# Kernel tuning notes

Hardware: AMD Instinct MI355X
Metric: run time of the kernel (lower is better)

The kernel has to match this reference:

```python
import jax, jax.numpy as jnp
import numpy as np

PATCH = 8

def setup_inputs() -> dict:
    key = jax.random.key(0)
    k0, k1, k2, k3 = jax.random.split(key, 4)
    dim = 128
    hidden = int(dim * 3)
    B, H, W = 4, 256, 256
    x = jax.random.normal(k0, (B, dim, H, W), jnp.float32)
    # project_in: Conv2d(dim, 2*hidden, k=1, bias=False) -> weight [2h, dim]
    w_in = jax.random.normal(k1, (2 * hidden, dim), jnp.float32) * 0.02
    # dwconv: Conv2d(2h, 2h, k=3, groups=2h) -> depthwise kernel [2h, 1, 3, 3]
    w_dw = jax.random.normal(k2, (2 * hidden, 1, 3, 3), jnp.float32) * 0.1
    # spectral filter, initialized to ones as in the module
    fft_filter = jnp.ones((dim, 1, 1, PATCH, PATCH // 2 + 1), jnp.float32)
    # project_out: Conv2d(hidden, dim, k=1) -> weight [dim, hidden]
    w_out = jax.random.normal(k3, (dim, hidden), jnp.float32) * 0.02
    return {"x": x, "w_in": w_in, "w_dw": w_dw, "fft_filter": fft_filter, "w_out": w_out}


def reference(x, w_in, w_dw, fft_filter, w_out):
    P = PATCH
    # 1x1 project_in: [B, dim, H, W] -> [B, 2h, H, W]
    h = jnp.einsum('oi,bihw->bohw', w_in, x)
    # 3x3 depthwise conv, SAME padding
    h = jax.lax.conv_general_dilated(
        h, w_dw, window_strides=(1, 1), padding='SAME',
        dimension_numbers=('NCHW', 'OIHW', 'NCHW'),
        feature_group_count=h.shape[1])
    x1, x2 = jnp.split(h, 2, axis=1)
    g = jax.nn.gelu(x1, approximate=False) * x2  # torch F.gelu is exact erf
    # 1x1 project_out: [B, hidden, H, W] -> [B, dim, H, W]
    y = jnp.einsum('oi,bihw->bohw', w_out, g)
    b, c, H, W = y.shape
    hn = (P - H % P) % P
    wn = (P - W % P) % P
    if hn or wn:
        y = jnp.pad(y, ((0, 0), (0, 0), (0, hn), (0, wn)), mode='reflect')
    Hp, Wp = y.shape[2], y.shape[3]
    # b c (h p1) (w p2) -> b c h w p1 p2
    yp = y.reshape(b, c, Hp // P, P, Wp // P, P).transpose(0, 1, 2, 4, 3, 5)
    yf = jnp.fft.rfft2(yp)                 # [b, c, h, w, P, P//2+1] complex
    yf = yf * fft_filter                   # broadcast over (c,1,1,P,P//2+1)
    yp = jnp.fft.irfft2(yf, s=(P, P))
    y = yp.transpose(0, 1, 2, 4, 3, 5).reshape(b, c, Hp, Wp)
    return y[:, :, :H, :W]
```

## Files before the change

### kernel.cpp

```cpp
#include <hip/hip_runtime.h>

typedef _Float16 f16;
typedef _Float16 f16x2 __attribute__((ext_vector_type(2)));
typedef _Float16 f16x4 __attribute__((ext_vector_type(4)));
typedef _Float16 f16x8 __attribute__((ext_vector_type(8)));
typedef __fp16  fp16x2 __attribute__((ext_vector_type(2)));
typedef float f32x4 __attribute__((ext_vector_type(4)));

#define DIM  128
#define HID  384
#define HID2 768
#define NPX  65536
#define NB   4

static __device__ __forceinline__ f16x2 bc2(unsigned u) {
    union { unsigned u; f16x2 h; } x; x.u = u; return x.h;
}

__global__ __launch_bounds__(256) void k_prep_w(
    const float* __restrict__ w_in, const float* __restrict__ w_out,
    const float* __restrict__ w_dw,
    f16* __restrict__ wibf, f16* __restrict__ wobf, f16* __restrict__ wpkT)
{
    int i = blockIdx.x * 256 + threadIdx.x;
    if (i < HID2 * DIM) {
        int j = i & 7, l = (i >> 3) & 63, ni = (i >> 9) & 3;
        int wn = (i >> 11) & 1, kk = (i >> 12) & 3, cN = i >> 14;
        int lr = l & 15, lh = l >> 4;
        int n = wn*64 + ni*16 + lr;
        int row = (n < 64) ? cN*64 + n : 384 + cN*64 + (n - 64);
        wibf[i] = (f16)w_in[row*128 + kk*32 + lh*8 + j];
    }
    if (i < DIM * HID) {
        int j = i & 7, l = (i >> 3) & 63, ni = (i >> 9) & 3;
        int wn = (i >> 11) & 1, kk2 = (i >> 12) & 1, cs = i >> 13;
        int lr = l & 15, lh = l >> 4;
        int ch_out = wn*64 + ni*16 + lr;
        int ch_in  = cs*64 + kk2*32 + lh*8 + j;
        wobf[i] = (f16)w_out[ch_out*HID + ch_in];
    }
    if (i < 9 * HID2) {
        int k = i / HID2, ch = i - k * HID2;
        wpkT[i] = (f16)w_dw[ch * 9 + k];
    }
}

__global__ void k_ktab(const float* __restrict__ filt, float* __restrict__ ktab,
                       int* __restrict__ isdelta)
{
    int c = blockIdx.x, t = threadIdx.x;
    int a = t >> 3, bb = t & 7;
    const float ct[8] = {1.f, 0.70710678118654752f, 0.f, -0.70710678118654752f,
                        -1.f, -0.70710678118654752f, 0.f, 0.70710678118654752f};
    float s = 0.f;
    for (int u = 0; u < 8; ++u)
        for (int v = 0; v < 8; ++v) {
            float Guv = (v <= 4) ? filt[c*40 + u*5 + v]
                                 : filt[c*40 + ((8-u)&7)*5 + (8-v)];
            s += Guv * ct[(u*a + v*bb) & 7];
        }
    s *= (1.f/64.f);
    ktab[c*64 + t] = s;
    float want = (t == 0) ? 1.f : 0.f;
    unsigned long long m = __ballot(fabsf(s - want) < 1e-5f);
    if (t == 0) isdelta[c] = (m == 0xFFFFFFFFFFFFFFFFULL) ? 1 : 0;
}

__global__ __launch_bounds__(256) void k_transpose(
    const float* __restrict__ x, f16* __restrict__ xt)
{
    __shared__ float tile[64][65];
    const int b = blockIdx.z;
    const float* xb = x + (size_t)b * DIM * NPX;
    f16* xtb = xt + (size_t)b * NPX * DIM;
    const int c0 = blockIdx.y * 64, p0 = blockIdx.x * 64;
    for (int i = threadIdx.x; i < 4096; i += 256) {
        int cl = i >> 6, pl = i & 63;
        tile[pl][cl] = xb[(size_t)(c0+cl)*NPX + p0 + pl];
    }
    __syncthreads();
    for (int i = threadIdx.x; i < 2048; i += 256) {
        int pl = i >> 5, c2 = (i & 31) * 2;
        f16x2 v = { (f16)tile[pl][c2], (f16)tile[pl][c2+1] };
        *(f16x2*)&xtb[(size_t)(p0+pl)*DIM + c0 + c2] = v;
    }
}

__global__ __launch_bounds__(256, 2) void k_fused(
    const f16* __restrict__ xt, const f16* __restrict__ wibf,
    const f16* __restrict__ wobf, const f16* __restrict__ wpkT,
    const float* __restrict__ ktab, const int* __restrict__ isdelta,
    float* __restrict__ out)
{
    __shared__ __attribute__((aligned(16))) char uni[33792];
    __shared__ f16 h1s[64*132];
    __shared__ f16 h2s[64*132];
    __shared__ f16 gAs[64*64];
    f16*   As = (f16*)uni;
    float* yl = (float*)uni;

    const int t  = threadIdx.x;
    const int tx = (blockIdx.x & 31) * 8;
    const int ty = (blockIdx.x >> 5) * 8;
    const f16* xtb = xt + (size_t)blockIdx.y * NPX * DIM;
    float* outb = out + (size_t)blockIdx.y * DIM * NPX;

#pragma unroll
    for (int j = 0; j < 8; ++j) {
        int i = t + j*256;
        int m = i >> 4, c8 = i & 15;
        int hr = (m * 683) >> 13;
        int hc = m - hr*12;
        int gy = ty - 1 + hr, gx = tx - 1 + hc;
        f16x8 v = {0,0,0,0,0,0,0,0};
        if (hr < 10 && hc < 10 && (unsigned)gy < 256u && (unsigned)gx < 256u)
            v = *(const f16x8*)&xtb[(size_t)(gy*256 + gx)*DIM + c8*8];
        *(f16x8*)&As[(m*128 + c8*8) ^ ((m & 7) << 3)] = v;
    }
    __syncthreads();

    const int l = t & 63, w = t >> 6, lr = l & 15, lh = l >> 4;
    const int wm = w >> 1, wn = w & 1;
    const int sch = t & 63;
    const int spy = (t >> 6) * 2;

    unsigned Ap[4][6], Up[4][4];
    f16x2 w2[9];
    f16x2 acc2a[2][4], acc2b[2][4];
    f32x4 accY[2][4];
#pragma unroll
    for (int mi = 0; mi < 2; ++mi)
#pragma unroll
        for (int ni = 0; ni < 4; ++ni) accY[mi][ni] = (f32x4){0.f,0.f,0.f,0.f};

#define STEN_LOAD(HB, CHOFF)                                                     \
    { _Pragma("unroll")                                                          \
      for (int r = 0; r < 4; ++r) {                                              \
        const f16* rp = &HB[sch*132 + (spy + r)*12];                             \
        uint2 q0 = *(const uint2*)(rp);                                          \
        uint2 q1 = *(const uint2*)(rp + 4);                                      \
        uint2 q2 = *(const uint2*)(rp + 8);                                      \
        Ap[r][0]=q0.x; Ap[r][1]=q0.y; Ap[r][2]=q1.x;                             \
        Ap[r][3]=q1.y; Ap[r][4]=q2.x; Ap[r][5]=q2.y;                             \
        Up[r][0]=__builtin_amdgcn_alignbit(Ap[r][1],Ap[r][0],16);                \
        Up[r][1]=__builtin_amdgcn_alignbit(Ap[r][2],Ap[r][1],16);                \
        Up[r][2]=__builtin_amdgcn_alignbit(Ap[r][3],Ap[r][2],16);                \
        Up[r][3]=__builtin_amdgcn_alignbit(Ap[r][4],Ap[r][3],16);                \
      }                                                                          \
      _Pragma("unroll")                                                          \
      for (int k = 0; k < 9; ++k) {                                              \
        f16 wv = wpkT[k*HID2 + (CHOFF) + cs*64 + sch];                           \
        w2[k] = (f16x2){wv, wv};                                                 \
      } }

#define STEN_FMA(ACC2)                                                           \
    { _Pragma("unroll")                                                          \
      for (int rr = 0; rr < 2; ++rr) {                                           \
        _Pragma("unroll")                                                        \
        for (int j = 0; j < 4; ++j) ACC2[rr][j] = (f16x2){0,0};                  \
        _Pragma("unroll")                                                        \
        for (int dy = 0; dy < 3; ++dy) {                                         \
          int r = rr + dy;                                                       \
          _Pragma("unroll")                                                      \
          for (int j = 0; j < 4; ++j) {                                          \
            ACC2[rr][j] = __builtin_elementwise_fma(bc2(Ap[r][j]),   w2[dy*3+0], ACC2[rr][j]); \
            ACC2[rr][j] = __builtin_elementwise_fma(bc2(Up[r][j]),   w2[dy*3+1], ACC2[rr][j]); \
            ACC2[rr][j] = __builtin_elementwise_fma(bc2(Ap[r][j+1]), w2[dy*3+2], ACC2[rr][j]); \
          } } } }

#define GATE_GA()                                                                \
    { _Pragma("unroll")                                                          \
      for (int rr = 0; rr < 2; ++rr) {                                           \
        const int oy = spy + rr;                                                 \
        _Pragma("unroll")                                                        \
        for (int j = 0; j < 4; ++j) {                                            \
          _Pragma("unroll")                                                      \
          for (int hf = 0; hf < 2; ++hf) {                                       \
            float av_ = (float)acc2a[rr][j][hf];                                 \
            float bv_ = (float)acc2b[rr][j][hf];                                 \
            float z  = av_ * 0.70710678118654752f;                               \
            float z2 = z * z;                                                    \
            float er = z * (1.1283791671f + z2*(-0.3761263890f                   \
                         + z2*0.1128379167f));                                   \
            er = fminf(1.0f, fmaxf(-1.0f, er));                                  \
            float ge = 0.5f * av_ * (1.0f + er);                                 \
            int jx = j*2 + hf;                                                   \
            gAs[(oy*8 + jx)*64 + (sch ^ (jx << 3))] = (f16)(ge * bv_);           \
          } } } }

#define GEMM2(CS)                                                                \
    { _Pragma("unroll")                                                          \
      for (int kk2 = 0; kk2 < 2; ++kk2) {                                        \
        f16x8 a2[2], b2[4];                                                      \
        _Pragma("unroll")                                                        \
        for (int mi = 0; mi < 2; ++mi) {                                         \
          int row = wm*32 + mi*16 + lr;                                          \
          a2[mi] = *(const f16x8*)&gAs[row*64 + ((kk2*32 + lh*8) ^ ((row&7)<<3))]; \
        }                                                                        \
        _Pragma("unroll")                                                        \
        for (int ni = 0; ni < 4; ++ni)                                           \
          b2[ni] = *(const f16x8*)&wobf[(((((CS)*2 + kk2)*2 + wn)*4 + ni)*64 + l)*8]; \
        _Pragma("unroll")                                                        \
        for (int mi = 0; mi < 2; ++mi)                                           \
          _Pragma("unroll")                                                      \
          for (int ni = 0; ni < 4; ++ni)                                         \
            accY[mi][ni] = __builtin_amdgcn_mfma_f32_16x16x32_f16(               \
                a2[mi], b2[ni], accY[mi][ni], 0, 0, 0);                          \
      } }

    for (int cN = 0; cN < 6; ++cN) {
        const bool doS = (cN > 0);
        const int  cs  = cN - 1;

        f32x4 acc[4][4];
#pragma unroll
        for (int mi = 0; mi < 4; ++mi)
#pragma unroll
            for (int ni = 0; ni < 4; ++ni) acc[mi][ni] = (f32x4){0.f,0.f,0.f,0.f};

#pragma unroll
        for (int kk = 0; kk < 4; ++kk) {
            f16x8 avf[4], bvf[4];
#pragma unroll
            for (int mi = 0; mi < 4; ++mi) {
                int r = wm*64 + mi*16 + lr;
                avf[mi] = *(const f16x8*)&As[(r*128 + kk*32 + lh*8) ^ ((r & 7) << 3)];
            }
#pragma unroll
            for (int ni = 0; ni < 4; ++ni)
                bvf[ni] = *(const f16x8*)
                    &wibf[((((cN*4 + kk)*2 + wn)*4 + ni)*64 + l) * 8];
            __builtin_amdgcn_s_setprio(1);
#pragma unroll
            for (int mi = 0; mi < 4; ++mi)
#pragma unroll
                for (int ni = 0; ni < 4; ++ni)
                    acc[mi][ni] = __builtin_amdgcn_mfma_f32_16x16x32_f16(
                        avf[mi], bvf[ni], acc[mi][ni], 0, 0, 0);
            __builtin_amdgcn_s_setprio(0);

            if (doS) {
                if (kk == 0) { STEN_LOAD(h1s, 0) }
                if (kk == 1) { STEN_FMA(acc2a) }
                if (kk == 2) { STEN_LOAD(h2s, HID) }
                if (kk == 3) { STEN_FMA(acc2b) }
            }
        }
        if (doS) { GATE_GA() }

        __syncthreads();
        if (doS) { GEMM2(cs) }

        {
            f16* hb = (wn == 0) ? h1s : h2s;
#pragma unroll
            for (int mi = 0; mi < 4; ++mi)
#pragma unroll
                for (int ni = 0; ni < 4; ++ni) {
                    int ch = ni*16 + lr;
                    int m  = wm*64 + mi*16 + lh*4;
                    union { struct { fp16x2 a, b; } p; f16x4 v; } u;
                    u.p.a = __builtin_amdgcn_cvt_pkrtz(acc[mi][ni][0], acc[mi][ni][1]);
                    u.p.b = __builtin_amdgcn_cvt_pkrtz(acc[mi][ni][2], acc[mi][ni][3]);
                    *(f16x4*)&hb[ch*132 + m] = u.v;
                }
        }
        __syncthreads();
    }

    {
        const int cs = 5;
        STEN_LOAD(h1s, 0)
        STEN_FMA(acc2a)
        STEN_LOAD(h2s, HID)
        STEN_FMA(acc2b)
        GATE_GA()
        __syncthreads();
        GEMM2(5)
    }

#pragma unroll
    for (int mi = 0; mi < 2; ++mi)
#pragma unroll
        for (int ni = 0; ni < 4; ++ni) {
            int ch = wn*64 + ni*16 + lr;
#pragma unroll
            for (int r = 0; r < 4; ++r) {
                int px = wm*32 + mi*16 + lh*4 + r;
                yl[px*132 + ch] = accY[mi][ni][r];
            }
        }
    __syncthreads();

    const int c = t & 127, half = t >> 7;
    if (isdelta[c]) {
#pragma unroll
        for (int r = 0; r < 4; ++r) {
            int pl = half*4 + r;
            float o0[8];
#pragma unroll
            for (int xx = 0; xx < 8; ++xx) o0[xx] = yl[(pl*8 + xx)*132 + c];
            size_t ob = (size_t)c*NPX + (size_t)(ty + pl)*256 + tx;
            *(float4*)&outb[ob]     = make_float4(o0[0], o0[1], o0[2], o0[3]);
            *(float4*)&outb[ob + 4] = make_float4(o0[4], o0[5], o0[6], o0[7]);
        }
    } else {
        const float* kc = &ktab[c*64];
        for (int r = 0; r < 4; ++r) {
            int pyl = half*4 + r;
            float o0[8];
            for (int xx = 0; xx < 8; ++xx) {
                float s = 0.f;
                for (int a = 0; a < 8; ++a)
                    for (int bb = 0; bb < 8; ++bb)
                        s += kc[a*8 + bb] *
                             yl[(((pyl - a) & 7)*8 + ((xx - bb) & 7))*132 + c];
                o0[xx] = s;
            }
            size_t ob = (size_t)c*NPX + (size_t)(ty + pyl)*256 + tx;
            *(float4*)&outb[ob]     = make_float4(o0[0], o0[1], o0[2], o0[3]);
            *(float4*)&outb[ob + 4] = make_float4(o0[4], o0[5], o0[6], o0[7]);
        }
    }
#undef STEN_LOAD
#undef STEN_FMA
#undef GATE_GA
#undef GEMM2
}

__global__ void k_diag(float* out, float v) { out[0] = v; }

extern "C" void kernel_launch(void* const* d_in, const int* in_sizes, int n_in,
                              void* d_out, int out_size, void* d_ws, size_t ws_size,
                              hipStream_t stream)
{
    const float* x     = (const float*)d_in[0];
    const float* w_in  = (const float*)d_in[1];
    const float* w_dw  = (const float*)d_in[2];
    const float* filt  = (const float*)d_in[3];
    const float* w_out = (const float*)d_in[4];
    float* out = (float*)d_out;
    char* ws = (char*)d_ws;

    const size_t OFF_WIB = 0;
    const size_t OFF_WOB = 196608;
    const size_t OFF_KT  = OFF_WOB + 98304;
    const size_t OFF_ISD = OFF_KT + 32768;
    const size_t OFF_WPK = OFF_ISD + 512;
    const size_t WEND    = 524288;

    const size_t SZ_XT = (size_t)NB * NPX * DIM * 2;
    const size_t NEED  = WEND + SZ_XT;
    if (ws_size < NEED) {
        k_diag<<<1, 1, 0, stream>>>(out, (float)((double)ws_size / 1048576.0));
        return;
    }

    f16*   wibf = (f16*)(ws + OFF_WIB);
    f16*   wobf = (f16*)(ws + OFF_WOB);
    float* kt   = (float*)(ws + OFF_KT);
    int*   isd  = (int*)(ws + OFF_ISD);
    f16*   wpk  = (f16*)(ws + OFF_WPK);
    f16*   xt   = (f16*)(ws + WEND);

    k_prep_w<<<dim3(384), dim3(256), 0, stream>>>(w_in, w_out, w_dw, wibf, wobf, wpk);
    k_ktab<<<dim3(128), dim3(64), 0, stream>>>(filt, kt, isd);
    k_transpose<<<dim3(1024, 2, NB), dim3(256), 0, stream>>>(x, xt);
    k_fused<<<dim3(1024, NB), dim3(256), 0, stream>>>(xt, wibf, wobf, wpk, kt, isd, out);
}
```

Measured before the change: 359.8 us.

## Double fused kernel block to 512 threads with finer per-wave work split

Raises the fused kernel to 512 threads (8 waves) per block. Each wave now computes half the output columns of the GEMM tiles, one stencil output row and fewer accumulators, so register pressure drops and more waves can hide latency. The h1s/h2s row pitch is padded from 132 to 134 to change LDS bank mapping. Block indices are swizzled so consecutive blocks cover spread-out tiles. The cost is more waves each doing less MFMA work and reloading the same A fragments, plus larger barriers.

```diff
diff --git a/kernel.cpp b/kernel.cpp
--- a/kernel.cpp
+++ b/kernel.cpp
@@ -86,28 +86,30 @@
     }
 }
 
-__global__ __launch_bounds__(256, 2) void k_fused(
+__global__ __launch_bounds__(512, 4) void k_fused(
     const f16* __restrict__ xt, const f16* __restrict__ wibf,
     const f16* __restrict__ wobf, const f16* __restrict__ wpkT,
     const float* __restrict__ ktab, const int* __restrict__ isdelta,
     float* __restrict__ out)
 {
     __shared__ __attribute__((aligned(16))) char uni[33792];
-    __shared__ f16 h1s[64*132];
-    __shared__ f16 h2s[64*132];
+    __shared__ f16 h1s[64*134];
+    __shared__ f16 h2s[64*134];
     __shared__ f16 gAs[64*64];
     f16*   As = (f16*)uni;
     float* yl = (float*)uni;
 
     const int t  = threadIdx.x;
-    const int tx = (blockIdx.x & 31) * 8;
-    const int ty = (blockIdx.x >> 5) * 8;
+    const int bid = blockIdx.x;
+    const int swz = (bid & 7) * 128 + (bid >> 3);
+    const int tx = (swz & 31) * 8;
+    const int ty = (swz >> 5) * 8;
     const f16* xtb = xt + (size_t)blockIdx.y * NPX * DIM;
     float* outb = out + (size_t)blockIdx.y * DIM * NPX;
 
 #pragma unroll
-    for (int j = 0; j < 8; ++j) {
-        int i = t + j*256;
+    for (int j = 0; j < 4; ++j) {
+        int i = t + j*512;
         int m = i >> 4, c8 = i & 15;
         int hr = (m * 683) >> 13;
         int hc = m - hr*12;
@@ -120,23 +122,23 @@
     __syncthreads();
 
     const int l = t & 63, w = t >> 6, lr = l & 15, lh = l >> 4;
-    const int wm = w >> 1, wn = w & 1;
+    const int wm = w >> 2, wn4 = w & 3;
     const int sch = t & 63;
-    const int spy = (t >> 6) * 2;
-
-    unsigned Ap[4][6], Up[4][4];
+    const int spy = w;
+
+    unsigned Ap[3][6], Up[3][4];
     f16x2 w2[9];
-    f16x2 acc2a[2][4], acc2b[2][4];
-    f32x4 accY[2][4];
+    f16x2 acc2a[4], acc2b[4];
+    f32x4 accY[2][2];
 #pragma unroll
     for (int mi = 0; mi < 2; ++mi)
 #pragma unroll
-        for (int ni = 0; ni < 4; ++ni) accY[mi][ni] = (f32x4){0.f,0.f,0.f,0.f};
+        for (int ni = 0; ni < 2; ++ni) accY[mi][ni] = (f32x4){0.f,0.f,0.f,0.f};
 
 #define STEN_LOAD(HB, CHOFF)                                                     \
     { _Pragma("unroll")                                                          \
-      for (int r = 0; r < 4; ++r) {                                              \
-        const f16* rp = &HB[sch*132 + (spy + r)*12];                             \
+      for (int r = 0; r < 3; ++r) {                                              \
+        const f16* rp = &HB[sch*134 + (spy + r)*12];                             \
         uint2 q0 = *(const uint2*)(rp);                                          \
         uint2 q1 = *(const uint2*)(rp + 4);                                      \
         uint2 q2 = *(const uint2*)(rp + 8);                                      \
@@ -155,55 +157,52 @@
 
 #define STEN_FMA(ACC2)                                                           \
     { _Pragma("unroll")                                                          \
-      for (int rr = 0; rr < 2; ++rr) {                                           \
-        _Pragma("unroll")                                                        \
-        for (int j = 0; j < 4; ++j) ACC2[rr][j] = (f16x2){0,0};                  \
-        _Pragma("unroll")                                                        \
-        for (int dy = 0; dy < 3; ++dy) {                                         \
-          int r = rr + dy;                                                       \
-          _Pragma("unroll")                                                      \
-          for (int j = 0; j < 4; ++j) {                                          \
-            ACC2[rr][j] = __builtin_elementwise_fma(bc2(Ap[r][j]),   w2[dy*3+0], ACC2[rr][j]); \
-            ACC2[rr][j] = __builtin_elementwise_fma(bc2(Up[r][j]),   w2[dy*3+1], ACC2[rr][j]); \
-            ACC2[rr][j] = __builtin_elementwise_fma(bc2(Ap[r][j+1]), w2[dy*3+2], ACC2[rr][j]); \
-          } } } }
+      for (int j = 0; j < 4; ++j) ACC2[j] = (f16x2){0,0};                        \
+      _Pragma("unroll")                                                          \
+      for (int dy = 0; dy < 3; ++dy) {                                           \
+        _Pragma("unroll")                                                        \
+        for (int j = 0; j < 4; ++j) {                                            \
+          ACC2[j] = __builtin_elementwise_fma(bc2(Ap[dy][j]),   w2[dy*3+0], ACC2[j]); \
+          ACC2[j] = __builtin_elementwise_fma(bc2(Up[dy][j]),   w2[dy*3+1], ACC2[j]); \
+          ACC2[j] = __builtin_elementwise_fma(bc2(Ap[dy][j+1]), w2[dy*3+2], ACC2[j]); \
+        } } }
 
 #define GATE_GA()                                                                \
     { _Pragma("unroll")                                                          \
-      for (int rr = 0; rr < 2; ++rr) {                                           \
-        const int oy = spy + rr;                                                 \
-        _Pragma("unroll")                                                        \
-        for (int j = 0; j < 4; ++j) {                                            \
-          _Pragma("unroll")                                                      \
-          for (int hf = 0; hf < 2; ++hf) {                                       \
-            float av_ = (float)acc2a[rr][j][hf];                                 \
-            float bv_ = (float)acc2b[rr][j][hf];                                 \
-            float z  = av_ * 0.70710678118654752f;                               \
-            float z2 = z * z;                                                    \
-            float er = z * (1.1283791671f + z2*(-0.3761263890f                   \
-                         + z2*0.1128379167f));                                   \
-            er = fminf(1.0f, fmaxf(-1.0f, er));                                  \
-            float ge = 0.5f * av_ * (1.0f + er);                                 \
-            int jx = j*2 + hf;                                                   \
-            gAs[(oy*8 + jx)*64 + (sch ^ (jx << 3))] = (f16)(ge * bv_);           \
-          } } } }
+      for (int j = 0; j < 4; ++j) {                                              \
+        _Pragma("unroll")                                                        \
+        for (int hf = 0; hf < 2; ++hf) {                                         \
+          float av_ = (float)acc2a[j][hf];                                       \
+          float bv_ = (float)acc2b[j][hf];                                       \
+          float z  = av_ * 0.70710678118654752f;                                 \
+          float z2 = z * z;                                                      \
+          float er = z * (1.1283791671f + z2*(-0.3761263890f                     \
+                       + z2*0.1128379167f));                                     \
+          er = fminf(1.0f, fmaxf(-1.0f, er));                                    \
+          float ge = 0.5f * av_ * (1.0f + er);                                   \
+          int jx = j*2 + hf;                                                     \
+          gAs[(spy*8 + jx)*64 + (sch ^ (jx << 3))] = (f16)(ge * bv_);            \
+        } } }
 
 #define GEMM2(CS)                                                                \
     { _Pragma("unroll")                                                          \
       for (int kk2 = 0; kk2 < 2; ++kk2) {                                        \
-        f16x8 a2[2], b2[4];                                                      \
+        f16x8 a2[2], b2[2];                                                      \
         _Pragma("unroll")                                                        \
         for (int mi = 0; mi < 2; ++mi) {                                         \
           int row = wm*32 + mi*16 + lr;                                          \
           a2[mi] = *(const f16x8*)&gAs[row*64 + ((kk2*32 + lh*8) ^ ((row&7)<<3))]; \
         }                                                                        \
         _Pragma("unroll")                                                        \
-        for (int ni = 0; ni < 4; ++ni)                                           \
-          b2[ni] = *(const f16x8*)&wobf[(((((CS)*2 + kk2)*2 + wn)*4 + ni)*64 + l)*8]; \
+        for (int ni = 0; ni < 2; ++ni) {                                         \
+          int nt = wn4*2 + ni;                                                   \
+          b2[ni] = *(const f16x8*)                                               \
+              &wobf[(((((CS)*2 + kk2)*2 + (nt>>2))*4 + (nt&3))*64 + l)*8];       \
+        }                                                                        \
         _Pragma("unroll")                                                        \
         for (int mi = 0; mi < 2; ++mi)                                           \
           _Pragma("unroll")                                                      \
-          for (int ni = 0; ni < 4; ++ni)                                         \
+          for (int ni = 0; ni < 2; ++ni)                                         \
             accY[mi][ni] = __builtin_amdgcn_mfma_f32_16x16x32_f16(               \
                 a2[mi], b2[ni], accY[mi][ni], 0, 0, 0);                          \
       } }
@@ -212,29 +211,31 @@
         const bool doS = (cN > 0);
         const int  cs  = cN - 1;
 
-        f32x4 acc[4][4];
+        f32x4 acc[4][2];
 #pragma unroll
         for (int mi = 0; mi < 4; ++mi)
 #pragma unroll
-            for (int ni = 0; ni < 4; ++ni) acc[mi][ni] = (f32x4){0.f,0.f,0.f,0.f};
+            for (int ni = 0; ni < 2; ++ni) acc[mi][ni] = (f32x4){0.f,0.f,0.f,0.f};
 
 #pragma unroll
         for (int kk = 0; kk < 4; ++kk) {
-            f16x8 avf[4], bvf[4];
+            f16x8 avf[4], bvf[2];
 #pragma unroll
             for (int mi = 0; mi < 4; ++mi) {
                 int r = wm*64 + mi*16 + lr;
                 avf[mi] = *(const f16x8*)&As[(r*128 + kk*32 + lh*8) ^ ((r & 7) << 3)];
             }
 #pragma unroll
-            for (int ni = 0; ni < 4; ++ni)
+            for (int ni = 0; ni < 2; ++ni) {
+                int nt = wn4*2 + ni;
                 bvf[ni] = *(const f16x8*)
-                    &wibf[((((cN*4 + kk)*2 + wn)*4 + ni)*64 + l) * 8];
+                    &wibf[((((cN*4 + kk)*2 + (nt>>2))*4 + (nt&3))*64 + l) * 8];
+            }
             __builtin_amdgcn_s_setprio(1);
 #pragma unroll
             for (int mi = 0; mi < 4; ++mi)
 #pragma unroll
-                for (int ni = 0; ni < 4; ++ni)
+                for (int ni = 0; ni < 2; ++ni)
                     acc[mi][ni] = __builtin_amdgcn_mfma_f32_16x16x32_f16(
                         avf[mi], bvf[ni], acc[mi][ni], 0, 0, 0);
             __builtin_amdgcn_s_setprio(0);
@@ -252,17 +253,17 @@
         if (doS) { GEMM2(cs) }
 
         {
-            f16* hb = (wn == 0) ? h1s : h2s;
+            f16* hb = (wn4 < 2) ? h1s : h2s;
 #pragma unroll
             for (int mi = 0; mi < 4; ++mi)
 #pragma unroll
-                for (int ni = 0; ni < 4; ++ni) {
-                    int ch = ni*16 + lr;
+                for (int ni = 0; ni < 2; ++ni) {
+                    int ch = (wn4 & 1)*32 + ni*16 + lr;
                     int m  = wm*64 + mi*16 + lh*4;
                     union { struct { fp16x2 a, b; } p; f16x4 v; } u;
                     u.p.a = __builtin_amdgcn_cvt_pkrtz(acc[mi][ni][0], acc[mi][ni][1]);
                     u.p.b = __builtin_amdgcn_cvt_pkrtz(acc[mi][ni][2], acc[mi][ni][3]);
-                    *(f16x4*)&hb[ch*132 + m] = u.v;
+                    *(f16x4*)&hb[ch*134 + m] = u.v;
                 }
         }
         __syncthreads();
@@ -282,8 +283,8 @@
 #pragma unroll
     for (int mi = 0; mi < 2; ++mi)
 #pragma unroll
-        for (int ni = 0; ni < 4; ++ni) {
-            int ch = wn*64 + ni*16 + lr;
+        for (int ni = 0; ni < 2; ++ni) {
+            int ch = wn4*32 + ni*16 + lr;
 #pragma unroll
             for (int r = 0; r < 4; ++r) {
                 int px = wm*32 + mi*16 + lh*4 + r;
@@ -292,11 +293,11 @@
         }
     __syncthreads();
 
-    const int c = t & 127, half = t >> 7;
+    const int c = t & 127, slot = t >> 7;
     if (isdelta[c]) {
 #pragma unroll
-        for (int r = 0; r < 4; ++r) {
-            int pl = half*4 + r;
+        for (int r = 0; r < 2; ++r) {
+            int pl = slot*2 + r;
             float o0[8];
 #pragma unroll
             for (int xx = 0; xx < 8; ++xx) o0[xx] = yl[(pl*8 + xx)*132 + c];
@@ -306,8 +307,8 @@
         }
     } else {
         const float* kc = &ktab[c*64];
-        for (int r = 0; r < 4; ++r) {
-            int pyl = half*4 + r;
+        for (int r = 0; r < 2; ++r) {
+            int pyl = slot*2 + r;
             float o0[8];
             for (int xx = 0; xx < 8; ++xx) {
                 float s = 0.f;
@@ -366,5 +367,5 @@
     k_prep_w<<<dim3(384), dim3(256), 0, stream>>>(w_in, w_out, w_dw, wibf, wobf, wpk);
     k_ktab<<<dim3(128), dim3(64), 0, stream>>>(filt, kt, isd);
     k_transpose<<<dim3(1024, 2, NB), dim3(256), 0, stream>>>(x, xt);
-    k_fused<<<dim3(1024, NB), dim3(256), 0, stream>>>(xt, wibf, wobf, wpk, kt, isd, out);
-}
+    k_fused<<<dim3(1024, NB), dim3(512), 0, stream>>>(xt, wibf, wobf, wpk, kt, isd, out);
+}
```

Result: slower. 938.2 us (+160.8%).
